# Kernel optimization log

Measured on AMD Instinct MI355X. Metric: run time of the kernel, lower is better.

Reference implementation:

```python
import jax, jax.numpy as jnp
import numpy as np
import math

D_MODEL, N_HEADS, N_LEVELS, N_POINTS = 256, 8, 4, 4
SPATIAL = [(80, 80), (40, 40), (20, 20), (10, 10)]


def setup_inputs() -> dict:
    key = jax.random.key(0)
    ks = jax.random.split(key, 8)
    N = 1
    C, H, L, P = D_MODEL, N_HEADS, N_LEVELS, N_POINTS
    shapes = np.array(SPATIAL, np.int32)
    len_in = int((shapes[:, 0] * shapes[:, 1]).sum())  # 8500
    Lq = len_in  # encoder self-attention: queries == flattened pixels
    start = np.concatenate([[0], np.cumsum(shapes[:, 0] * shapes[:, 1])[:-1]]).astype(np.int32)

    query = jax.random.normal(ks[0], (N, Lq, C), jnp.float32)
    reference_points = jax.random.uniform(ks[1], (N, Lq, L, 2), dtype=jnp.float32)
    input_flatten = jax.random.normal(ks[2], (N, len_in, C), jnp.float32)

    # sampling_offsets bias: grid init as in _reset_parameters
    thetas = jnp.arange(H, dtype=jnp.float32) * (2.0 * math.pi / H)
    grid = jnp.stack([jnp.cos(thetas), jnp.sin(thetas)], -1)
    grid = grid / jnp.max(jnp.abs(grid), axis=-1, keepdims=True)
    grid = jnp.tile(grid[:, None, None, :], (1, L, P, 1)) * jnp.arange(1, P + 1, dtype=jnp.float32)[None, None, :, None]
    b_off = grid.reshape(-1)
    W_off = jax.random.normal(ks[3], (C, H * L * P * 2), jnp.float32) * 0.01
    W_attn = jax.random.normal(ks[4], (C, H * L * P), jnp.float32) * 0.01
    b_attn = jnp.zeros((H * L * P,), jnp.float32)
    s = 1.0 / np.sqrt(C)
    W_v = jax.random.normal(ks[5], (C, C), jnp.float32) * s
    b_v = jnp.zeros((C,), jnp.float32)
    W_out = jax.random.normal(ks[6], (C, C), jnp.float32) * s
    b_out = jnp.zeros((C,), jnp.float32)
    return {
        "query": query, "reference_points": reference_points, "input_flatten": input_flatten,
        "input_spatial_shapes": jnp.asarray(shapes), "input_level_start_index": jnp.asarray(start),
        "W_off": W_off, "b_off": b_off, "W_attn": W_attn, "b_attn": b_attn,
        "W_v": W_v, "b_v": b_v, "W_out": W_out, "b_out": b_out,
    }


def _ms_deform_core(value, spatial_shapes, level_start_index, loc, attn):
    # value: (N, Len_in, H, d); loc: (N, Lq, H, L, P, 2) normalized [0,1]; attn: (N, Lq, H, L, P)
    N, Len_in, H, d = value.shape
    _, Lq, _, L, P, _ = loc.shape
    Hi = spatial_shapes[:, 0][None, None, None, :, None]  # (1,1,1,L,1)
    Wi = spatial_shapes[:, 1][None, None, None, :, None]
    # grid_sample(align_corners=False) semantics used by the CUDA ms_deform_attn kernel
    x = loc[..., 0] * Wi.astype(loc.dtype) - 0.5  # (N,Lq,H,L,P)
    y = loc[..., 1] * Hi.astype(loc.dtype) - 0.5
    x0 = jnp.floor(x); y0 = jnp.floor(y)
    lw = x - x0; lh = y - y0
    x0i = x0.astype(jnp.int32); y0i = y0.astype(jnp.int32)
    v = value.transpose(0, 2, 1, 3)  # (N,H,Len_in,d)
    start = level_start_index[None, None, None, :, None]
    out = jnp.zeros((N, Lq, H, d), value.dtype)
    corners = [(0, 0, (1 - lh) * (1 - lw)), (0, 1, (1 - lh) * lw),
               (1, 0, lh * (1 - lw)), (1, 1, lh * lw)]
    for dy, dx, wgt in corners:
        hc = y0i + dy; wc = x0i + dx
        valid = (hc >= 0) & (hc < Hi) & (wc >= 0) & (wc < Wi)
        idx = start + jnp.clip(hc, 0, Hi - 1) * Wi + jnp.clip(wc, 0, Wi - 1)  # (N,Lq,H,L,P)
        w = jnp.where(valid, wgt, 0.0) * attn  # (N,Lq,H,L,P)
        idx_g = idx.transpose(0, 2, 1, 3, 4).reshape(N, H, Lq * L * P)
        sampled = jnp.take_along_axis(v, idx_g[..., None], axis=2)  # (N,H,Lq*L*P,d)
        sampled = sampled.reshape(N, H, Lq, L, P, d)
        out = out + jnp.einsum('nhqlpd,nqhlp->nqhd', sampled, w)
    return out.reshape(N, Lq, H * d)


def reference(query, reference_points, input_flatten, input_spatial_shapes, input_level_start_index,
              W_off, b_off, W_attn, b_attn, W_v, b_v, W_out, b_out):
    N, Lq, C = query.shape
    H, L, P = N_HEADS, N_LEVELS, N_POINTS
    d = C // H
    value = (input_flatten @ W_v + b_v).reshape(N, -1, H, d)
    off = (query @ W_off + b_off).reshape(N, Lq, H, L, P, 2)
    attn = jax.nn.softmax((query @ W_attn + b_attn).reshape(N, Lq, H, L * P), axis=-1)
    attn = attn.reshape(N, Lq, H, L, P)
    # reference_points last dim == 2 branch
    norm = jnp.stack([input_spatial_shapes[:, 1], input_spatial_shapes[:, 0]], -1).astype(query.dtype)  # (L,2) = (W,H)
    loc = reference_points[:, :, None, :, None, :] + off / norm[None, None, None, :, None, :]
    out = _ms_deform_core(value, input_spatial_shapes, input_level_start_index, loc, attn)
    return out @ W_out + b_out
```

## Files before the change

kernel.cpp:

```cpp
#include <hip/hip_runtime.h>

#define LQ    8500
#define C_DIM 256

typedef __attribute__((ext_vector_type(8))) short bf16x8;
typedef __attribute__((ext_vector_type(4))) float f32x4;

__device__ __forceinline__ unsigned short f2bf(float x) {
    union { float f; unsigned u; } c; c.f = x;
    unsigned r = c.u + 0x7FFFu + ((c.u >> 16) & 1u);
    return (unsigned short)(r >> 16);
}
__device__ __forceinline__ float bf2f(unsigned us) {
    union { unsigned u; float f; } c; c.u = us << 16;
    return c.f;
}

__device__ __forceinline__ void gload_lds16(const void* g, void* l) {
    __builtin_amdgcn_global_load_lds(
        (const __attribute__((address_space(1))) unsigned int*)g,
        (__attribute__((address_space(3))) unsigned int*)l, 16, 0, 0);
}

__global__ __launch_bounds__(256)
void prep_all(const float* __restrict__ query, const float* __restrict__ inflat,
              const float* __restrict__ Wv,   const float* __restrict__ Wout,
              const float* __restrict__ Woff, const float* __restrict__ Wattn,
              const float* __restrict__ boff, const float* __restrict__ battn,
              unsigned short* __restrict__ qbf,  unsigned short* __restrict__ ibf,
              unsigned short* __restrict__ Wv_t, unsigned short* __restrict__ Wout_t,
              unsigned short* __restrict__ Wcat_t, float* __restrict__ bcat)
{
    const int NV = LQ * 256 / 8;
    const int tid    = blockIdx.x * 256 + threadIdx.x;
    const int stride = gridDim.x * 256;

    for (int v = tid; v < 2 * NV; v += stride) {
        const float*    src = (v < NV) ? query + (size_t)v * 8 : inflat + (size_t)(v - NV) * 8;
        unsigned short* dst = (v < NV) ? qbf   + (size_t)v * 8 : ibf    + (size_t)(v - NV) * 8;
        const float4 f0 = ((const float4*)src)[0];
        const float4 f1 = ((const float4*)src)[1];
        bf16x8 o;
        o[0] = (short)f2bf(f0.x); o[1] = (short)f2bf(f0.y);
        o[2] = (short)f2bf(f0.z); o[3] = (short)f2bf(f0.w);
        o[4] = (short)f2bf(f1.x); o[5] = (short)f2bf(f1.y);
        o[6] = (short)f2bf(f1.z); o[7] = (short)f2bf(f1.w);
        *(bf16x8*)dst = o;
    }

    const int total = 65536 * 3 + 32768 + 384;
    for (int i = tid; i < total; i += stride) {
        if (i < 65536) {
            int k = i >> 8, n = i & 255;
            Wv_t[n * 256 + k] = f2bf(Wv[i]);
        } else if (i < 131072) {
            int j = i - 65536; int k = j >> 8, n = j & 255;
            Wout_t[n * 256 + k] = f2bf(Wout[j]);
        } else if (i < 196608) {
            int j = i - 131072; int k = j >> 8, n = j & 255;
            Wcat_t[n * 256 + k] = f2bf(Woff[j]);
        } else if (i < 229376) {
            int j = i - 196608; int k = j >> 7, n = j & 127;
            Wcat_t[(256 + n) * 256 + k] = f2bf(Wattn[j]);
        } else {
            int j = i - 229376;
            bcat[j] = (j < 256) ? boff[j] : battn[j - 256];
        }
    }
}

template<int OUTMODE, int NJ>
__device__ __forceinline__ void gemm_body(
    const unsigned short* __restrict__ A, const unsigned short* __restrict__ Bt,
    const float* __restrict__ bias, void* __restrict__ Out,
    int M, int N, int r0, int c0,
    char* As, char* Bs)
{
    const int t    = threadIdx.x;
    const int lane = t & 63, wave = t >> 6;
    const int wr   = wave >> 1, wc = wave & 1;
    const int lrow = lane & 15, lgrp = lane >> 4;
    constexpr int BROWS = NJ * 32;
    constexpr int BBUF  = BROWS * 128;

    f32x4 acc[2][NJ] = {};

    auto stage = [&](int buf, int k0) {
#pragma unroll
        for (int r = 0; r < 2; ++r) {
            const int row   = r * 32 + (t >> 3);
            const int chunk = (t & 7) ^ (row & 7);
            const unsigned short* g =
                A + (size_t)min(r0 + row, M - 1) * 256 + k0 + chunk * 8;
            gload_lds16(g, As + buf * 8192 + r * 4096 + wave * 1024);
        }
#pragma unroll
        for (int r = 0; r < BROWS / 32; ++r) {
            const int row   = r * 32 + (t >> 3);
            const int chunk = (t & 7) ^ (row & 7);
            const unsigned short* g = Bt + (size_t)(c0 + row) * 256 + k0 + chunk * 8;
            gload_lds16(g, Bs + buf * BBUF + r * 4096 + wave * 1024);
        }
    };

    auto compute = [&](int buf) {
#pragma unroll
        for (int kk = 0; kk < 2; ++kk) {
            const int g = kk * 4 + lgrp;
            bf16x8 a[2], b[NJ];
#pragma unroll
            for (int mi = 0; mi < 2; ++mi) {
                const int row = wr * 32 + mi * 16 + lrow;
                a[mi] = *(const bf16x8*)(As + buf * 8192 + row * 128 +
                                         ((g ^ (row & 7)) * 16));
            }
#pragma unroll
            for (int nj = 0; nj < NJ; ++nj) {
                const int row = wc * (NJ * 16) + nj * 16 + lrow;
                b[nj] = *(const bf16x8*)(Bs + buf * BBUF + row * 128 +
                                         ((g ^ (row & 7)) * 16));
            }
#pragma unroll
            for (int mi = 0; mi < 2; ++mi)
#pragma unroll
                for (int nj = 0; nj < NJ; ++nj)
                    acc[mi][nj] = __builtin_amdgcn_mfma_f32_16x16x32_bf16(
                        a[mi], b[nj], acc[mi][nj], 0, 0, 0);
        }
    };

    stage(0, 0);
    __syncthreads();
    int cur = 0;
#pragma unroll
    for (int it = 0; it < 3; ++it) {
        stage(cur ^ 1, (it + 1) * 64);
        compute(cur);
        __syncthreads();
        cur ^= 1;
    }
    compute(cur);

#pragma unroll
    for (int mi = 0; mi < 2; ++mi)
#pragma unroll
        for (int nj = 0; nj < NJ; ++nj) {
            const int col = c0 + wc * (NJ * 16) + nj * 16 + lrow;
            const float bb = bias[col];
#pragma unroll
            for (int j = 0; j < 4; ++j) {
                const int row = r0 + wr * 32 + mi * 16 + lgrp * 4 + j;
                if (row < M) {
                    const float v = acc[mi][nj][j] + bb;
                    if constexpr (OUTMODE == 0)
                        ((float*)Out)[(size_t)row * N + col] = v;
                    else if constexpr (OUTMODE == 1)
                        ((unsigned short*)Out)[(size_t)row * N + col] = f2bf(v);
                    else
                        ((unsigned short*)Out)[(size_t)(col >> 5) * (LQ * 32) +
                                               (size_t)row * 32 + (col & 31)] = f2bf(v);
                }
            }
        }
}

__global__ __launch_bounds__(256)
void gemm_dual(const unsigned short* __restrict__ A0, const unsigned short* __restrict__ B0,
               const float* __restrict__ bias0, unsigned short* __restrict__ out0,
               const unsigned short* __restrict__ A1, const unsigned short* __restrict__ B1,
               const float* __restrict__ bias1, unsigned short* __restrict__ out1)
{
    __shared__ __align__(16) char As[2 * 64 * 64 * 2];
    __shared__ __align__(16) char Bs[2 * 128 * 64 * 2];
    const int orig = blockIdx.x;
    const int xcd  = orig & 7, pos = orig >> 3;
    const int wgid = (xcd == 0 ? 0 : 84 + (xcd - 1) * 83) + pos;
    const int r0 = (wgid / 5) * 64;
    const int c  = wgid % 5;
    if (c < 2)
        gemm_body<2, 4>(A0, B0, bias0, out0, LQ, 256, r0, c * 128, As, Bs);
    else
        gemm_body<1, 4>(A1, B1, bias1, out1, LQ, 384, r0, (c - 2) * 128, As, Bs);
}

__global__ __launch_bounds__(256)
void gemm_f32out(const unsigned short* __restrict__ A, const unsigned short* __restrict__ Bt,
                 const float* __restrict__ bias, float* __restrict__ out)
{
    __shared__ __align__(16) char As[2 * 64 * 64 * 2];
    __shared__ __align__(16) char Bs[2 * 64 * 64 * 2];
    const int orig = blockIdx.x;
    const int xcd  = orig & 7, pos = orig >> 3;
    const int wgid = (xcd < 4 ? xcd * 67 : 268 + (xcd - 4) * 66) + pos;
    gemm_body<0, 2>(A, Bt, bias, out, LQ, 256, (wgid >> 2) * 64, (wgid & 3) * 64,
                    As, Bs);
}

template<int J>
__device__ __forceinline__ void gather_j(const char* vb,
                                         const int* c_off, const float* c_w,
                                         float* a)
{
#pragma unroll
    for (int corner = 0; corner < 4; ++corner) {
        const int bo = __builtin_amdgcn_mov_dpp(c_off[corner], J * 0x55, 0xf, 0xf, 0);
        union { int i; float f; } uw;
        union { float f; int i; } sw; sw.f = c_w[corner];
        uw.i = __builtin_amdgcn_mov_dpp(sw.i, J * 0x55, 0xf, 0xf, 0);
        const float w = uw.f;
        const uint4 v = *(const uint4*)(vb + (size_t)(unsigned)bo);
        a[0] = fmaf(w, bf2f(v.x & 0xffffu), a[0]);
        a[1] = fmaf(w, bf2f(v.x >> 16), a[1]);
        a[2] = fmaf(w, bf2f(v.y & 0xffffu), a[2]);
        a[3] = fmaf(w, bf2f(v.y >> 16), a[3]);
        a[4] = fmaf(w, bf2f(v.z & 0xffffu), a[4]);
        a[5] = fmaf(w, bf2f(v.z >> 16), a[5]);
        a[6] = fmaf(w, bf2f(v.w & 0xffffu), a[6]);
        a[7] = fmaf(w, bf2f(v.w >> 16), a[7]);
    }
}

__global__ __launch_bounds__(256)
void msda_sample(const unsigned short* __restrict__ value,
                 const unsigned short* __restrict__ offattn,
                 const float* __restrict__ refp,
                 const int*   __restrict__ shapes,
                 const int*   __restrict__ lstart,
                 unsigned short* __restrict__ msda)
{
    const int orig = blockIdx.x;
    const int xcd  = orig & 7, pos = orig >> 3;
    const int wgid = (xcd < 2 ? xcd * 532 : 1064 + (xcd - 2) * 531) + pos;

    const int t   = threadIdx.x;
    const int sub = t >> 7, tl = t & 127;
    const int q   = wgid * 2 + sub;

    int   c_off[4];
    float c_w[4];
    {
        const int lp = tl & 15, l = lp >> 2;
        const int Hs = shapes[2 * l + 0];
        const int Ws = shapes[2 * l + 1];
        const int st = lstart[l];

        const unsigned oxy = *(const unsigned*)(offattn + (size_t)q * 384 + 2 * tl);
        const float ox = bf2f(oxy & 0xffffu);
        const float oy = bf2f(oxy >> 16);
        const float rx = refp[q * 8 + l * 2 + 0];
        const float ry = refp[q * 8 + l * 2 + 1];

        const float x = (rx + ox / (float)Ws) * (float)Ws - 0.5f;
        const float y = (ry + oy / (float)Hs) * (float)Hs - 0.5f;
        const float x0f = floorf(x), y0f = floorf(y);
        const float lw = x - x0f, lh = y - y0f;
        const int   x0 = (int)x0f, y0 = (int)y0f;

        const float logit = bf2f(offattn[(size_t)q * 384 + 256 + tl]);
        float m = logit;
        for (int s = 8; s >= 1; s >>= 1) m = fmaxf(m, __shfl_xor(m, s, 16));
        const float e = __expf(logit - m);
        float ssum = e;
        for (int s = 8; s >= 1; s >>= 1) ssum += __shfl_xor(ssum, s, 16);
        const float a = e / ssum;

#pragma unroll
        for (int corner = 0; corner < 4; ++corner) {
            const int dy = corner >> 1, dx = corner & 1;
            const int hc = y0 + dy, wc = x0 + dx;
            const bool valid = (hc >= 0) && (hc < Hs) && (wc >= 0) && (wc < Ws);
            const float wy = dy ? lh : (1.f - lh);
            const float wx = dx ? lw : (1.f - lw);
            const int hcc = min(max(hc, 0), Hs - 1);
            const int wcc = min(max(wc, 0), Ws - 1);
            c_off[corner] = (st + hcc * Ws + wcc) * 64;
            c_w[corner]   = valid ? (wy * wx * a) : 0.f;
        }
    }

    const int chunk = tl & 3, quarter = (tl >> 2) & 3, h = tl >> 4;
    const char* vb = (const char*)value + (size_t)h * (LQ * 64) + chunk * 16;
    float a[8] = {0.f, 0.f, 0.f, 0.f, 0.f, 0.f, 0.f, 0.f};
    gather_j<0>(vb, c_off, c_w, a);
    gather_j<1>(vb, c_off, c_w, a);
    gather_j<2>(vb, c_off, c_w, a);
    gather_j<3>(vb, c_off, c_w, a);

#pragma unroll
    for (int i = 0; i < 8; ++i) {
        a[i] += __shfl_xor(a[i], 4);
        a[i] += __shfl_xor(a[i], 8);
    }
    if (quarter == 0) {
        uint4 o;
        o.x = (unsigned)f2bf(a[0]) | ((unsigned)f2bf(a[1]) << 16);
        o.y = (unsigned)f2bf(a[2]) | ((unsigned)f2bf(a[3]) << 16);
        o.z = (unsigned)f2bf(a[4]) | ((unsigned)f2bf(a[5]) << 16);
        o.w = (unsigned)f2bf(a[6]) | ((unsigned)f2bf(a[7]) << 16);
        *(uint4*)(msda + (size_t)q * 256 + h * 32 + chunk * 8) = o;
    }
}

extern "C" void kernel_launch(void* const* d_in, const int* in_sizes, int n_in,
                              void* d_out, int out_size, void* d_ws, size_t ws_size,
                              hipStream_t stream)
{
    const float* query  = (const float*)d_in[0];
    const float* refp   = (const float*)d_in[1];
    const float* inflat = (const float*)d_in[2];
    const int*   shapes = (const int*)  d_in[3];
    const int*   lstart = (const int*)  d_in[4];
    const float* W_off  = (const float*)d_in[5];
    const float* b_off  = (const float*)d_in[6];
    const float* W_attn = (const float*)d_in[7];
    const float* b_attn = (const float*)d_in[8];
    const float* W_v    = (const float*)d_in[9];
    const float* b_v    = (const float*)d_in[10];
    const float* W_out  = (const float*)d_in[11];
    const float* b_out  = (const float*)d_in[12];

    float* out = (float*)d_out;
    char*  ws  = (char*)d_ws;

    size_t o = 0;
    unsigned short* qbf    = (unsigned short*)(ws + o); o += (size_t)LQ * 256 * 2;
    unsigned short* ibf    = (unsigned short*)(ws + o); o += (size_t)LQ * 256 * 2;
    unsigned short* Wv_t   = (unsigned short*)(ws + o); o += 131072;
    unsigned short* Wout_t = (unsigned short*)(ws + o); o += 131072;
    unsigned short* Wcat_t = (unsigned short*)(ws + o); o += 196608;
    float*          bcat   = (float*)         (ws + o); o += 1536;
    unsigned short* value  = (unsigned short*)(ws + o); o += (size_t)LQ * 256 * 2;
    unsigned short* offattn= (unsigned short*)(ws + o); o += (size_t)LQ * 384 * 2;
    unsigned short* msda   = (unsigned short*)(ws + o);

    prep_all<<<1024, 256, 0, stream>>>(query, inflat, W_v, W_out, W_off, W_attn,
                                       b_off, b_attn, qbf, ibf,
                                       Wv_t, Wout_t, Wcat_t, bcat);

    gemm_dual<<<665, 256, 0, stream>>>(ibf, Wv_t, b_v, value,
                                       qbf, Wcat_t, bcat, offattn);

    msda_sample<<<4250, 256, 0, stream>>>(value, offattn, refp, shapes, lstart, msda);

    gemm_f32out<<<532, 256, 0, stream>>>(msda, Wout_t, b_out, out);
}
```

Measured before the change: 48.64 us.

## Fuse deformable sampling with output projection GEMM via LDS tile

```diff
diff --git a/kernel.cpp b/kernel.cpp
--- a/kernel.cpp
+++ b/kernel.cpp
@@ -152,9 +152,7 @@
                 const int row = r0 + wr * 32 + mi * 16 + lgrp * 4 + j;
                 if (row < M) {
                     const float v = acc[mi][nj][j] + bb;
-                    if constexpr (OUTMODE == 0)
-                        ((float*)Out)[(size_t)row * N + col] = v;
-                    else if constexpr (OUTMODE == 1)
+                    if constexpr (OUTMODE == 1)
                         ((unsigned short*)Out)[(size_t)row * N + col] = f2bf(v);
                     else
                         ((unsigned short*)Out)[(size_t)(col >> 5) * (LQ * 32) +
@@ -181,19 +179,6 @@
         gemm_body<2, 4>(A0, B0, bias0, out0, LQ, 256, r0, c * 128, As, Bs);
     else
         gemm_body<1, 4>(A1, B1, bias1, out1, LQ, 384, r0, (c - 2) * 128, As, Bs);
-}
-
-__global__ __launch_bounds__(256)
-void gemm_f32out(const unsigned short* __restrict__ A, const unsigned short* __restrict__ Bt,
-                 const float* __restrict__ bias, float* __restrict__ out)
-{
-    __shared__ __align__(16) char As[2 * 64 * 64 * 2];
-    __shared__ __align__(16) char Bs[2 * 64 * 64 * 2];
-    const int orig = blockIdx.x;
-    const int xcd  = orig & 7, pos = orig >> 3;
-    const int wgid = (xcd < 4 ? xcd * 67 : 268 + (xcd - 4) * 66) + pos;
-    gemm_body<0, 2>(A, Bt, bias, out, LQ, 256, (wgid >> 2) * 64, (wgid & 3) * 64,
-                    As, Bs);
 }
 
 template<int J>
@@ -220,84 +205,121 @@
     }
 }
 
-__global__ __launch_bounds__(256)
-void msda_sample(const unsigned short* __restrict__ value,
-                 const unsigned short* __restrict__ offattn,
-                 const float* __restrict__ refp,
-                 const int*   __restrict__ shapes,
-                 const int*   __restrict__ lstart,
-                 unsigned short* __restrict__ msda)
-{
+__global__ __launch_bounds__(512)
+void msda_out(const unsigned short* __restrict__ value,
+              const unsigned short* __restrict__ offattn,
+              const float* __restrict__ refp,
+              const int*   __restrict__ shapes,
+              const int*   __restrict__ lstart,
+              const unsigned short* __restrict__ Wout_t,
+              const float* __restrict__ b_out,
+              float* __restrict__ out)
+{
+    __shared__ __align__(16) char msda_lds[16 * 528];
+
     const int orig = blockIdx.x;
     const int xcd  = orig & 7, pos = orig >> 3;
-    const int wgid = (xcd < 2 ? xcd * 532 : 1064 + (xcd - 2) * 531) + pos;
+    const int wgid = (xcd < 4 ? xcd * 67 : 268 + (xcd - 4) * 66) + pos;
+    const int q0 = wgid * 16;
 
     const int t   = threadIdx.x;
-    const int sub = t >> 7, tl = t & 127;
-    const int q   = wgid * 2 + sub;
-
-    int   c_off[4];
-    float c_w[4];
-    {
-        const int lp = tl & 15, l = lp >> 2;
-        const int Hs = shapes[2 * l + 0];
-        const int Ws = shapes[2 * l + 1];
-        const int st = lstart[l];
-
-        const unsigned oxy = *(const unsigned*)(offattn + (size_t)q * 384 + 2 * tl);
-        const float ox = bf2f(oxy & 0xffffu);
-        const float oy = bf2f(oxy >> 16);
-        const float rx = refp[q * 8 + l * 2 + 0];
-        const float ry = refp[q * 8 + l * 2 + 1];
-
-        const float x = (rx + ox / (float)Ws) * (float)Ws - 0.5f;
-        const float y = (ry + oy / (float)Hs) * (float)Hs - 0.5f;
-        const float x0f = floorf(x), y0f = floorf(y);
-        const float lw = x - x0f, lh = y - y0f;
-        const int   x0 = (int)x0f, y0 = (int)y0f;
-
-        const float logit = bf2f(offattn[(size_t)q * 384 + 256 + tl]);
-        float m = logit;
-        for (int s = 8; s >= 1; s >>= 1) m = fmaxf(m, __shfl_xor(m, s, 16));
-        const float e = __expf(logit - m);
-        float ssum = e;
-        for (int s = 8; s >= 1; s >>= 1) ssum += __shfl_xor(ssum, s, 16);
-        const float a = e / ssum;
-
-#pragma unroll
-        for (int corner = 0; corner < 4; ++corner) {
-            const int dy = corner >> 1, dx = corner & 1;
-            const int hc = y0 + dy, wc = x0 + dx;
-            const bool valid = (hc >= 0) && (hc < Hs) && (wc >= 0) && (wc < Ws);
-            const float wy = dy ? lh : (1.f - lh);
-            const float wx = dx ? lw : (1.f - lw);
-            const int hcc = min(max(hc, 0), Hs - 1);
-            const int wcc = min(max(wc, 0), Ws - 1);
-            c_off[corner] = (st + hcc * Ws + wcc) * 64;
-            c_w[corner]   = valid ? (wy * wx * a) : 0.f;
-        }
-    }
-
+    const int grp = t >> 7, tl = t & 127;
     const int chunk = tl & 3, quarter = (tl >> 2) & 3, h = tl >> 4;
-    const char* vb = (const char*)value + (size_t)h * (LQ * 64) + chunk * 16;
-    float a[8] = {0.f, 0.f, 0.f, 0.f, 0.f, 0.f, 0.f, 0.f};
-    gather_j<0>(vb, c_off, c_w, a);
-    gather_j<1>(vb, c_off, c_w, a);
-    gather_j<2>(vb, c_off, c_w, a);
-    gather_j<3>(vb, c_off, c_w, a);
-
-#pragma unroll
-    for (int i = 0; i < 8; ++i) {
-        a[i] += __shfl_xor(a[i], 4);
-        a[i] += __shfl_xor(a[i], 8);
-    }
-    if (quarter == 0) {
-        uint4 o;
-        o.x = (unsigned)f2bf(a[0]) | ((unsigned)f2bf(a[1]) << 16);
-        o.y = (unsigned)f2bf(a[2]) | ((unsigned)f2bf(a[3]) << 16);
-        o.z = (unsigned)f2bf(a[4]) | ((unsigned)f2bf(a[5]) << 16);
-        o.w = (unsigned)f2bf(a[6]) | ((unsigned)f2bf(a[7]) << 16);
-        *(uint4*)(msda + (size_t)q * 256 + h * 32 + chunk * 8) = o;
+
+#pragma unroll
+    for (int it = 0; it < 4; ++it) {
+        const int qlocal = it * 4 + grp;
+        const int q = min(q0 + qlocal, LQ - 1);
+
+        int   c_off[4];
+        float c_w[4];
+        {
+            const int lp = tl & 15, l = lp >> 2;
+            const int Hs = shapes[2 * l + 0];
+            const int Ws = shapes[2 * l + 1];
+            const int st = lstart[l];
+
+            const unsigned oxy = *(const unsigned*)(offattn + (size_t)q * 384 + 2 * tl);
+            const float ox = bf2f(oxy & 0xffffu);
+            const float oy = bf2f(oxy >> 16);
+            const float rx = refp[q * 8 + l * 2 + 0];
+            const float ry = refp[q * 8 + l * 2 + 1];
+
+            const float x = (rx + ox / (float)Ws) * (float)Ws - 0.5f;
+            const float y = (ry + oy / (float)Hs) * (float)Hs - 0.5f;
+            const float x0f = floorf(x), y0f = floorf(y);
+            const float lw = x - x0f, lh = y - y0f;
+            const int   x0 = (int)x0f, y0 = (int)y0f;
+
+            const float logit = bf2f(offattn[(size_t)q * 384 + 256 + tl]);
+            float m = logit;
+            for (int s = 8; s >= 1; s >>= 1) m = fmaxf(m, __shfl_xor(m, s, 16));
+            const float e = __expf(logit - m);
+            float ssum = e;
+            for (int s = 8; s >= 1; s >>= 1) ssum += __shfl_xor(ssum, s, 16);
+            const float a = e / ssum;
+
+#pragma unroll
+            for (int corner = 0; corner < 4; ++corner) {
+                const int dy = corner >> 1, dx = corner & 1;
+                const int hc = y0 + dy, wc = x0 + dx;
+                const bool valid = (hc >= 0) && (hc < Hs) && (wc >= 0) && (wc < Ws);
+                const float wy = dy ? lh : (1.f - lh);
+                const float wx = dx ? lw : (1.f - lw);
+                const int hcc = min(max(hc, 0), Hs - 1);
+                const int wcc = min(max(wc, 0), Ws - 1);
+                c_off[corner] = (st + hcc * Ws + wcc) * 64;
+                c_w[corner]   = valid ? (wy * wx * a) : 0.f;
+            }
+        }
+
+        const char* vb = (const char*)value + (size_t)h * (LQ * 64) + chunk * 16;
+        float a[8] = {0.f, 0.f, 0.f, 0.f, 0.f, 0.f, 0.f, 0.f};
+        gather_j<0>(vb, c_off, c_w, a);
+        gather_j<1>(vb, c_off, c_w, a);
+        gather_j<2>(vb, c_off, c_w, a);
+        gather_j<3>(vb, c_off, c_w, a);
+
+#pragma unroll
+        for (int i = 0; i < 8; ++i) {
+            a[i] += __shfl_xor(a[i], 4);
+            a[i] += __shfl_xor(a[i], 8);
+        }
+        if (quarter == 0) {
+            uint4 o;
+            o.x = (unsigned)f2bf(a[0]) | ((unsigned)f2bf(a[1]) << 16);
+            o.y = (unsigned)f2bf(a[2]) | ((unsigned)f2bf(a[3]) << 16);
+            o.z = (unsigned)f2bf(a[4]) | ((unsigned)f2bf(a[5]) << 16);
+            o.w = (unsigned)f2bf(a[6]) | ((unsigned)f2bf(a[7]) << 16);
+            *(uint4*)(msda_lds + qlocal * 528 + h * 64 + chunk * 16) = o;
+        }
+    }
+    __syncthreads();
+
+    const int lane = t & 63, wave = t >> 6;
+    const int lrow = lane & 15, lgrp = lane >> 4;
+    const int c0 = wave * 32;
+
+    f32x4 acc[2] = {};
+#pragma unroll
+    for (int ks = 0; ks < 8; ++ks) {
+        const bf16x8 af = *(const bf16x8*)(msda_lds + lrow * 528 + ks * 64 + lgrp * 16);
+#pragma unroll
+        for (int nj = 0; nj < 2; ++nj) {
+            const bf16x8 bf = *(const bf16x8*)(Wout_t +
+                (size_t)(c0 + nj * 16 + lrow) * 256 + ks * 32 + lgrp * 8);
+            acc[nj] = __builtin_amdgcn_mfma_f32_16x16x32_bf16(af, bf, acc[nj], 0, 0, 0);
+        }
+    }
+#pragma unroll
+    for (int nj = 0; nj < 2; ++nj) {
+        const int col = c0 + nj * 16 + lrow;
+        const float bb = b_out[col];
+#pragma unroll
+        for (int j = 0; j < 4; ++j) {
+            const int q = q0 + lgrp * 4 + j;
+            if (q < LQ) out[(size_t)q * 256 + col] = acc[nj][j] + bb;
+        }
     }
 }
 
@@ -331,7 +353,6 @@
     float*          bcat   = (float*)         (ws + o); o += 1536;
     unsigned short* value  = (unsigned short*)(ws + o); o += (size_t)LQ * 256 * 2;
     unsigned short* offattn= (unsigned short*)(ws + o); o += (size_t)LQ * 384 * 2;
-    unsigned short* msda   = (unsigned short*)(ws + o);
 
     prep_all<<<1024, 256, 0, stream>>>(query, inflat, W_v, W_out, W_off, W_attn,
                                        b_off, b_attn, qbf, ibf,
@@ -340,7 +361,6 @@
     gemm_dual<<<665, 256, 0, stream>>>(ibf, Wv_t, b_v, value,
                                        qbf, Wcat_t, bcat, offattn);
 
-    msda_sample<<<4250, 256, 0, stream>>>(value, offattn, refp, shapes, lstart, msda);
-
-    gemm_f32out<<<532, 256, 0, stream>>>(msda, Wout_t, b_out, out);
-}
+    msda_out<<<532, 512, 0, stream>>>(value, offattn, refp, shapes, lstart,
+                                      Wout_t, b_out, out);
+}
```

Result: slower. 60.21 us (+23.8%).
